# Optimization experiments

Hardware: AMD Instinct MI355X
Metric: run time of the kernel (lower is better)

## Reference

```python
import jax, jax.numpy as jnp
import numpy as np
from jax import lax

EPS = 1e-5
B, C, H, W = 16, 256, 56, 56
HEADS, DIM_K, DIM_U, DIM_OUT = 4, 16, 4, 256
DIM_V = DIM_OUT // HEADS  # 64
R = 15


def setup_inputs() -> dict:
    key = jax.random.key(0)
    ks = jax.random.split(key, 16)
    s = 0.05
    return {
        "x": jax.random.normal(ks[0], (B, C, H, W), jnp.float32),
        "Wq": jax.random.normal(ks[1], (C, HEADS * DIM_K), jnp.float32) * s,
        "Wk": jax.random.normal(ks[2], (C, DIM_U * DIM_K), jnp.float32) * s,
        "Wv": jax.random.normal(ks[3], (C, DIM_U * DIM_V), jnp.float32) * s,
        "pos_w": jax.random.normal(ks[4], (DIM_K, DIM_U, 1, R, R), jnp.float32) * s,
        "pos_b": jax.random.normal(ks[5], (DIM_K,), jnp.float32) * s,
        "gq": jax.random.uniform(ks[6], (HEADS * DIM_K,), jnp.float32),
        "bq": jax.random.normal(ks[7], (HEADS * DIM_K,), jnp.float32) * s,
        "mq": jax.random.normal(ks[8], (HEADS * DIM_K,), jnp.float32) * s,
        "vq": jax.random.uniform(ks[9], (HEADS * DIM_K,), jnp.float32) + 0.5,
        "gv": jax.random.uniform(ks[10], (DIM_U * DIM_V,), jnp.float32),
        "bv": jax.random.normal(ks[11], (DIM_U * DIM_V,), jnp.float32) * s,
        "mv": jax.random.normal(ks[12], (DIM_U * DIM_V,), jnp.float32) * s,
        "vv": jax.random.uniform(ks[13], (DIM_U * DIM_V,), jnp.float32) + 0.5,
    }


def _bn(x, gamma, beta, mean, var):
    # inference-mode BatchNorm over channel dim (axis=1), x: [b,c,h,w]
    inv = gamma / jnp.sqrt(var + EPS)
    return x * inv[None, :, None, None] + (beta - mean * inv)[None, :, None, None]


def reference(x, Wq, Wk, Wv, pos_w, pos_b, gq, bq, mq, vq, gv, bv, mv, vv):
    b, c, hh, ww = x.shape
    n = hh * ww
    h, dk, u, dv = HEADS, DIM_K, DIM_U, DIM_V
    # 1x1 convs (channels_first) == channel matmuls
    q = jnp.einsum('bchw,cd->bdhw', x, Wq)
    k = jnp.einsum('bchw,cd->bdhw', x, Wk)
    v = jnp.einsum('bchw,cd->bdhw', x, Wv)
    q = _bn(q, gq, bq, mq, vq)
    v = _bn(v, gv, bv, mv, vv)
    # rearranges: 'b (h k) hh ww -> b h k (hh ww)', 'b (u k) hh ww -> b u k n', 'b (u v) hh ww -> b u v n'
    q = q.reshape(b, h, dk, n)
    k = k.reshape(b, u, dk, n)
    v = v.reshape(b, u, dv, n)
    k = jax.nn.softmax(k, axis=-1)  # keras Softmax default axis=-1 (positions)
    # content lambda
    Lc = jnp.einsum('bukm,buvm->bkv', k, v)
    Yc = jnp.einsum('bhkn,bkv->bnhv', q, Lc)
    # position lambda: conv3d over (v,hh,ww) with kernel (1,r,r), pad spatial only
    v5 = v.reshape(b, u, dv, hh, ww)  # [N, C=u, D=v, H, W]
    p = R // 2
    Lp = lax.conv_general_dilated(
        v5, pos_w, window_strides=(1, 1, 1),
        padding=[(0, 0), (p, p), (p, p)],
        dimension_numbers=('NCDHW', 'OIDHW', 'NCDHW'))
    Lp = Lp + pos_b[None, :, None, None, None]  # [b, k, v, hh, ww]
    Lp = Lp.reshape(b, dk, dv, n)
    Yp = jnp.einsum('bhkn,bkvn->bnhv', q, Lp)
    Y = Yc + Yp  # [b, n, h, v]
    # 'b (hh ww) h v -> b (h v) hh ww'
    out = Y.reshape(b, hh, ww, h, dv).transpose(0, 3, 4, 1, 2).reshape(b, h * dv, hh, ww)
    return out
```

## Files before the change

kernel.cpp:

```cpp
#include <hip/hip_runtime.h>
#include <cstdint>
#include <cstddef>

#define NB   16
#define NC   256
#define NPIX 3136
#define NW   56
#define EPSV 1e-5f

#define BSTR     (384 * NPIX)
#define OFF_VP   (128 * NPIX)
#define VROWD    36
#define VPLANE   (56 * VROWD)
#define OFF_PARTB 917504

#define OFF_AB   0u
#define OFF_BNA  49152u
#define OFF_BNB  49536u
#define OFF_WT   49920u
#define OFF_KS   58112u
#define OFF_LC   59136u
#define OFF_Y    75520u

typedef short bf16x8 __attribute__((ext_vector_type(8)));
typedef float f32x4  __attribute__((ext_vector_type(4)));
typedef float f32x16 __attribute__((ext_vector_type(16)));

__device__ __forceinline__ uint32_t f2bf(float f) {
  uint32_t x = __float_as_uint(f);
  uint32_t r = x + 0x7fffu + ((x >> 16) & 1u);
  return r >> 16;
}
__device__ __forceinline__ uint32_t cvtpk(float lo, float hi) {
  uint32_t r;
  asm("v_cvt_pk_bf16_f32 %0, %1, %2" : "=v"(r) : "v"(lo), "v"(hi));
  return r;
}

__device__ __forceinline__ float fetchW(const float* Wq, const float* Wk,
                                        const float* Wv, int m, int c) {
  if (m < 64)  return Wq[c * 64 + m];
  if (m < 128) return Wk[c * 64 + (m - 64)];
  return Wv[c * 256 + (m - 128)];
}

__global__ void prep_kernel(const float* __restrict__ Wq, const float* __restrict__ Wk,
                            const float* __restrict__ Wv, const float* __restrict__ pos_w,
                            const float* __restrict__ gq, const float* __restrict__ bq,
                            const float* __restrict__ mq, const float* __restrict__ vq,
                            const float* __restrict__ gv, const float* __restrict__ bv,
                            const float* __restrict__ mv, const float* __restrict__ vv,
                            float* __restrict__ ws) {
  int d = blockIdx.x;
  int c = threadIdx.x;
  int i = d * 256 + c;
  if (i < 49152) {
    int dgt = i >> 12, rem = i & 4095;
    int kc = rem >> 8, rem2 = rem & 255;
    int lane = rem2 >> 2, dp = rem2 & 3;
    int m = dgt * 32 + (lane & 31);
    int k0 = kc * 16 + (lane >> 5) * 8 + dp * 2;
    float w0 = fetchW(Wq, Wk, Wv, m, k0);
    float w1 = fetchW(Wq, Wk, Wv, m, k0 + 1);
    ((uint32_t*)(ws + OFF_AB))[i] = f2bf(w0) | (f2bf(w1) << 16);
  }
  if (c == 0) {
    float sa, sb;
    if (d < 64)        { float inv = gq[d] / sqrtf(vq[d] + EPSV); sa = inv; sb = bq[d] - mq[d] * inv; }
    else if (d < 128)  { sa = 1.0f; sb = 0.0f; }
    else               { int j = d - 128; float inv = gv[j] / sqrtf(vv[j] + EPSV); sa = inv; sb = bv[j] - mv[j] * inv; }
    ws[OFF_BNA + d] = sa;
    ws[OFF_BNB + d] = sb;
  }
  if (i < 8192) {
    int chunk = i >> 8, rem = i & 255, lane = rem >> 2, dp = rem & 3;
    int quad = lane >> 4, k = lane & 15;
    int u = chunk >> 3, t = chunk & 7;
    int dh = 2 * t + (quad >> 1);
    int dwb = (quad & 1) * 8 + dp * 2;
    float w0 = (dh < 15 && dwb     < 15) ? pos_w[k * 900 + u * 225 + dh * 15 + dwb]     : 0.0f;
    float w1 = (dh < 15 && dwb + 1 < 15) ? pos_w[k * 900 + u * 225 + dh * 15 + dwb + 1] : 0.0f;
    ((uint32_t*)(ws + OFF_WT))[i] = f2bf(w0) | (f2bf(w1) << 16);
  }
  if (i < 1024) ws[OFF_KS + i] = 0.0f;
  for (int g = i; g < 4096 * 56; g += 98304) {
    int plane = g / 56, r = g - plane * 56;
    int bb = plane >> 8, d2 = plane & 255;
    uint32_t* row = (uint32_t*)(ws + OFF_Y) + (size_t)bb * BSTR + OFF_VP
                    + (size_t)d2 * VPLANE + r * VROWD;
    uint4 z; z.x = 0; z.y = 0; z.z = 0; z.w = 0;
    *(uint4*)(row)      = z;
    *(uint4*)(row + 32) = z;
  }
}

__launch_bounds__(256, 2)
__global__ void qkv_mfma(const float* __restrict__ x, const float* __restrict__ wsc,
                         float* __restrict__ Y) {
  __shared__ uint32_t X[64 * 128];
  __shared__ float BNs[768];
  int tid = threadIdx.x;
  int n0 = blockIdx.x * 64, b = blockIdx.y;
  for (int i = tid; i < 768; i += 256) BNs[i] = wsc[OFF_BNA + i];
  const size_t xb = (size_t)b * NC * NPIX;
#pragma unroll
  for (int it = 0; it < 4; ++it) {
    int n2 = tid & 31;
    int cp4 = it * 8 + (tid >> 5);
    const float* xp = x + xb + (size_t)(cp4 * 8) * NPIX + n0 + n2 * 2;
    float2 ld[8];
#pragma unroll
    for (int j = 0; j < 8; ++j) ld[j] = *(const float2*)(xp + (size_t)j * NPIX);
    uint4 ve, vo;
    ve.x = cvtpk(ld[0].x, ld[1].x);
    ve.y = cvtpk(ld[2].x, ld[3].x);
    ve.z = cvtpk(ld[4].x, ld[5].x);
    ve.w = cvtpk(ld[6].x, ld[7].x);
    vo.x = cvtpk(ld[0].y, ld[1].y);
    vo.y = cvtpk(ld[2].y, ld[3].y);
    vo.z = cvtpk(ld[4].y, ld[5].y);
    vo.w = cvtpk(ld[6].y, ld[7].y);
    int ne = 2 * n2, no = ne + 1;
    *(uint4*)(X + ne * 128 + ((cp4 ^ (ne & 31)) << 2)) = ve;
    *(uint4*)(X + no * 128 + ((cp4 ^ (no & 31)) << 2)) = vo;
  }
  __syncthreads();
  int lane = tid & 63, w = tid >> 6;
  int n31 = lane & 31, h5 = lane >> 5;
  f32x16 acc[3][2];
#pragma unroll
  for (int dt = 0; dt < 3; ++dt)
#pragma unroll
    for (int nt = 0; nt < 2; ++nt)
#pragma unroll
      for (int e = 0; e < 16; ++e) acc[dt][nt][e] = 0.0f;
  const uint4* AB = (const uint4*)(wsc + OFF_AB);
  if (w == 0) {
#pragma unroll 4
    for (int kc = 0; kc < 16; ++kc) {
      bf16x8 af[3];
#pragma unroll
      for (int dt = 0; dt < 3; ++dt) {
        union { uint4 q; bf16x8 v; } tmp;
        tmp.q = AB[(size_t)((dt * 16 + kc)) * 64 + lane];
        af[dt] = tmp.v;
      }
#pragma unroll
      for (int nt = 0; nt < 2; ++nt) {
        union { uint4 q; bf16x8 v; } bu;
        bu.q = *(const uint4*)(X + (nt * 32 + n31) * 128 + (((2 * kc + h5) ^ n31) << 2));
        acc[0][nt] = __builtin_amdgcn_mfma_f32_32x32x16_bf16(af[0], bu.v, acc[0][nt], 0, 0, 0);
        acc[1][nt] = __builtin_amdgcn_mfma_f32_32x32x16_bf16(af[1], bu.v, acc[1][nt], 0, 0, 0);
        acc[2][nt] = __builtin_amdgcn_mfma_f32_32x32x16_bf16(bu.v, af[2], acc[2][nt], 0, 0, 0);
      }
    }
  } else {
#pragma unroll 4
    for (int kc = 0; kc < 16; ++kc) {
      bf16x8 af[3];
#pragma unroll
      for (int dt = 0; dt < 3; ++dt) {
        union { uint4 q; bf16x8 v; } tmp;
        tmp.q = AB[(size_t)(((w * 3 + dt) * 16 + kc)) * 64 + lane];
        af[dt] = tmp.v;
      }
#pragma unroll
      for (int nt = 0; nt < 2; ++nt) {
        union { uint4 q; bf16x8 v; } bu;
        bu.q = *(const uint4*)(X + (nt * 32 + n31) * 128 + (((2 * kc + h5) ^ n31) << 2));
#pragma unroll
        for (int dt = 0; dt < 3; ++dt)
          acc[dt][nt] = __builtin_amdgcn_mfma_f32_32x32x16_bf16(bu.v, af[dt], acc[dt][nt], 0, 0, 0);
      }
    }
  }
  int prr[2][4], pcc[2][4];
#pragma unroll
  for (int nt = 0; nt < 2; ++nt)
#pragma unroll
    for (int j = 0; j < 4; ++j) {
      int pb = n0 + nt * 32 + 8 * j + 4 * h5;
      prr[nt][j] = pb / NW;
      pcc[nt][j] = pb - prr[nt][j] * NW;
    }
  if (w == 0) {
#pragma unroll
    for (int dt = 0; dt < 2; ++dt) {
      int dgt = dt;
      float sa[16], sb[16];
#pragma unroll
      for (int g = 0; g < 4; ++g) {
        *(float4*)(sa + g * 4) = *(const float4*)(BNs + dgt * 32 + g * 8 + h5 * 4);
        *(float4*)(sb + g * 4) = *(const float4*)(BNs + 384 + dgt * 32 + g * 8 + h5 * 4);
      }
#pragma unroll
      for (int nt = 0; nt < 2; ++nt) {
        int pix = n0 + nt * 32 + n31;
        uint2* qb2 = (uint2*)(Y + (size_t)b * BSTR);
#pragma unroll
        for (int g = 0; g < 4; ++g) {
          float y0 = fmaf(acc[dt][nt][4 * g + 0], sa[4 * g + 0], sb[4 * g + 0]);
          float y1 = fmaf(acc[dt][nt][4 * g + 1], sa[4 * g + 1], sb[4 * g + 1]);
          float y2 = fmaf(acc[dt][nt][4 * g + 2], sa[4 * g + 2], sb[4 * g + 2]);
          float y3 = fmaf(acc[dt][nt][4 * g + 3], sa[4 * g + 3], sb[4 * g + 3]);
          uint2 val;
          val.x = cvtpk(y0, y1);
          val.y = cvtpk(y2, y3);
          qb2[(size_t)(dgt * 8 + 2 * g + h5) * NPIX + pix] = val;
        }
      }
    }
    {
      float* kp = Y + ((size_t)(b * 384) + 64 + n31) * NPIX;
#pragma unroll
      for (int nt = 0; nt < 2; ++nt)
#pragma unroll
        for (int j = 0; j < 4; ++j) {
          float4 st;
          st.x = acc[2][nt][4 * j + 0];
          st.y = acc[2][nt][4 * j + 1];
          st.z = acc[2][nt][4 * j + 2];
          st.w = acc[2][nt][4 * j + 3];
          *(float4*)(kp + prr[nt][j] * NW + pcc[nt][j]) = st;
        }
    }
  } else {
    unsigned short* vp = (unsigned short*)(Y + (size_t)b * BSTR + OFF_VP);
#pragma unroll
    for (int dt = 0; dt < 3; ++dt) {
      int dgt = w * 3 + dt;
      if (dgt == 3) {
        float* kp = Y + ((size_t)(b * 384) + 96 + n31) * NPIX;
#pragma unroll
        for (int nt = 0; nt < 2; ++nt)
#pragma unroll
          for (int j = 0; j < 4; ++j) {
            float4 st;
            st.x = acc[dt][nt][4 * j + 0];
            st.y = acc[dt][nt][4 * j + 1];
            st.z = acc[dt][nt][4 * j + 2];
            st.w = acc[dt][nt][4 * j + 3];
            *(float4*)(kp + prr[nt][j] * NW + pcc[nt][j]) = st;
          }
      } else {
        int d2 = dgt * 32 + n31 - 128;
        float sa = BNs[dgt * 32 + n31];
        float sb2 = BNs[384 + dgt * 32 + n31];
        unsigned short* vpd = vp + (size_t)d2 * 4032;
#pragma unroll
        for (int nt = 0; nt < 2; ++nt)
#pragma unroll
          for (int j = 0; j < 4; ++j) {
            float y0 = fmaf(acc[dt][nt][4 * j + 0], sa, sb2);
            float y1 = fmaf(acc[dt][nt][4 * j + 1], sa, sb2);
            float y2 = fmaf(acc[dt][nt][4 * j + 2], sa, sb2);
            float y3 = fmaf(acc[dt][nt][4 * j + 3], sa, sb2);
            uint2 val;
            val.x = cvtpk(y0, y1);
            val.y = cvtpk(y2, y3);
            *(uint2*)(vpd + prr[nt][j] * 72 + 8 + pcc[nt][j]) = val;
          }
      }
    }
  }
}

__launch_bounds__(256)
__global__ void lc_mfma(float* __restrict__ Y, float* __restrict__ ws) {
  __shared__ float R[4096];
  __shared__ float Rs[64];
  int bx = blockIdx.x, u = blockIdx.y, b = blockIdx.z;
  int tid = threadIdx.x;
  int lane = tid & 63, w = tid >> 6;
  int col = lane & 15, quad = lane >> 4;
  int slot = bx * 4 + w;
  const float* krow = Y + ((size_t)(b * 384 + 64 + u * 16 + col)) * NPIX;
  const uint32_t* vpb = (const uint32_t*)(Y + (size_t)b * BSTR + OFF_VP)
                        + (size_t)(u * 64 + col) * VPLANE;
  f32x4 acc[4];
#pragma unroll
  for (int vt = 0; vt < 4; ++vt) acc[vt] = (f32x4){0.f, 0.f, 0.f, 0.f};
  float ssum = 0.0f;
  for (int c = slot; c < 126; c += 64) {
    int p0 = c * 32 + quad * 8;
    int row = p0 / 72;
    int pc = p0 - row * 72;
    bool valid = (unsigned)(pc - 8) < 56u;
    float4 k0, k1;
    if (valid) {
      const float* kp = krow + row * NW + pc - 8;
      k0 = *(const float4*)(kp);
      k1 = *(const float4*)(kp + 4);
    } else {
      k0.x = k0.y = k0.z = k0.w = -1e30f;
      k1 = k0;
    }
    float e0 = __expf(k0.x), e1 = __expf(k0.y), e2 = __expf(k0.z), e3 = __expf(k0.w);
    float e4 = __expf(k1.x), e5 = __expf(k1.y), e6 = __expf(k1.z), e7 = __expf(k1.w);
    ssum += (e0 + e1 + e2 + e3) + (e4 + e5 + e6 + e7);
    union { uint32_t d[4]; bf16x8 v; } kb;
    kb.d[0] = cvtpk(e0, e1);
    kb.d[1] = cvtpk(e2, e3);
    kb.d[2] = cvtpk(e4, e5);
    kb.d[3] = cvtpk(e6, e7);
    int vdw = c * 16 + quad * 4;
#pragma unroll
    for (int vt = 0; vt < 4; ++vt) {
      union { uint4 q; bf16x8 v; } vb;
      vb.q = *(const uint4*)(vpb + (size_t)(vt * 16) * VPLANE + vdw);
      acc[vt] = __builtin_amdgcn_mfma_f32_16x16x32_bf16(vb.v, kb.v, acc[vt], 0, 0, 0);
    }
  }
  ssum += __shfl_xor(ssum, 16);
  ssum += __shfl_xor(ssum, 32);
#pragma unroll
  for (int vt = 0; vt < 4; ++vt)
#pragma unroll
    for (int r = 0; r < 4; ++r)
      R[w * 1024 + vt * 256 + quad * 64 + r * 16 + col] = acc[vt][r];
  if (lane < 16) Rs[w * 16 + col] = ssum;
  __syncthreads();
  float* P = Y + (size_t)b * BSTR + OFF_PARTB + (size_t)(u * 16 + bx) * 1024;
  float4 s0 = *(const float4*)(R + tid * 4);
  float4 s1 = *(const float4*)(R + 1024 + tid * 4);
  float4 s2 = *(const float4*)(R + 2048 + tid * 4);
  float4 s3 = *(const float4*)(R + 3072 + tid * 4);
  float4 tot;
  tot.x = (s0.x + s1.x) + (s2.x + s3.x);
  tot.y = (s0.y + s1.y) + (s2.y + s3.y);
  tot.z = (s0.z + s1.z) + (s2.z + s3.z);
  tot.w = (s0.w + s1.w) + (s2.w + s3.w);
  *(float4*)(P + tid * 4) = tot;
  if (tid < 16)
    atomicAdd(&ws[OFF_KS + b * 64 + u * 16 + tid],
              (Rs[tid] + Rs[16 + tid]) + (Rs[32 + tid] + Rs[48 + tid]));
}

__global__ void lc_reduce(const float* __restrict__ Y, float* __restrict__ ws) {
  int i = blockIdx.x, b = blockIdx.y;
  int t = threadIdx.x;
  __shared__ float invS[64];
  if (t < 64) invS[t] = 1.0f / ws[OFF_KS + b * 64 + t];
  __syncthreads();
  int idx = i * 256 + t;
  int k = idx & 15;
  const float* P = Y + (size_t)b * BSTR + OFF_PARTB;
  float tot = 0.0f;
#pragma unroll
  for (int u = 0; u < 4; ++u) {
    float su = 0.0f;
#pragma unroll
    for (int s = 0; s < 16; ++s) su += P[(size_t)(u * 16 + s) * 1024 + idx];
    tot += su * invS[u * 16 + k];
  }
  ws[OFF_LC + (b * 16 + k) * 64 + (idx >> 4)] = tot;
}

#define ROWS    29
#define RSTR2   72
#define UPITCH2 2088
#define LDSW2   8352

template<int PPLO, int PPHI>
__device__ __forceinline__ void conv_accum(const uint32_t* __restrict__ S,
                                           const uint4* __restrict__ wt,
                                           int abase, int lane, f32x4* acc) {
#pragma unroll 1
  for (int u = 0; u < 4; ++u) {
    bf16x8 wf[8];
#pragma unroll
    for (int t = 0; t < 8; ++t) {
      union { uint4 q; bf16x8 v; } tmp;
      tmp.q = wt[(u * 8 + t) * 64 + lane];
      wf[t] = tmp.v;
    }
    int au = u * UPITCH2 + abase;
#pragma unroll
    for (int PP = PPLO; PP < PPHI; ++PP) {
      int a = au + PP * (2 * RSTR2);
      union { uint32_t u4[4]; bf16x8 v8; } bu;
      bu.u4[0] = S[a];     bu.u4[1] = S[a + 2];
      bu.u4[2] = S[a + 4]; bu.u4[3] = S[a + 6];
#pragma unroll
      for (int t = 0; t < 8; ++t) {
        int q = PP - t;
        if (q >= 0 && q < 7)
          acc[q] = __builtin_amdgcn_mfma_f32_16x16x32_bf16(wf[t], bu.v8, acc[q], 0, 0, 0);
      }
    }
  }
}

__launch_bounds__(512, 4)
__global__ void pos_lambda_mfma(const float* __restrict__ Y, const float* __restrict__ wsc,
                                const float* __restrict__ pos_b, float* __restrict__ out) {
  __shared__ __attribute__((aligned(16))) uint32_t S[LDSW2];
  int v = blockIdx.x, b = blockIdx.y, band = blockIdx.z;
  int rb = band * 14;
  int tid = threadIdx.x;
  const uint32_t* vpad = (const uint32_t*)(Y + (size_t)b * BSTR + OFF_VP);
  for (int ii = tid; ii < 1044; ii += 512) {
    int u = ii / 261;
    int rem = ii - u * 261;
    int row = rem / 9;
    int j3 = rem - row * 9;
    int gr = rb + row - 7;
    uint32_t d0 = 0, d1 = 0, d2 = 0, d3 = 0, d4 = 0;
    if ((unsigned)gr < (unsigned)NW) {
      const uint32_t* pr32 = vpad + (size_t)(u * 64 + v) * VPLANE + gr * VROWD + 4 * j3;
      uint4 q4 = *(const uint4*)pr32;
      d0 = q4.x; d1 = q4.y; d2 = q4.z; d3 = q4.w;
      d4 = pr32[4];
    }
    uint32_t* dst = S + u * UPITCH2 + row * RSTR2 + 8 * j3;
    uint4 w0, w1;
    w0.x = __builtin_amdgcn_alignbit(d1, d0, 16);  w0.y = d1;
    w0.z = __builtin_amdgcn_alignbit(d2, d1, 16);  w0.w = d2;
    w1.x = __builtin_amdgcn_alignbit(d3, d2, 16);  w1.y = d3;
    w1.z = __builtin_amdgcn_alignbit(d4, d3, 16);  w1.w = d4;
    *(uint4*)(dst)     = w0;
    *(uint4*)(dst + 4) = w1;
  }
  __syncthreads();
  int lane = tid & 63, wid = tid >> 6;
  int quad = lane >> 4, n = lane & 15;
  int dhp = quad >> 1;
  int ct = wid & 3, p = wid >> 2;
  int cb = (ct == 3) ? 40 : ct * 16;
  int sb = cb + n + (quad & 1) * 8;
  int abase = (p + dhp) * RSTR2 + sb;
  const uint4* wt = (const uint4*)(wsc + OFF_WT);
  float lcq[4];
#pragma unroll
  for (int r = 0; r < 4; ++r) {
    int k = quad * 4 + r;
    lcq[r] = wsc[OFF_LC + (b * 16 + k) * 64 + v] + pos_b[k];
  }
  f32x4 acc[7];
#pragma unroll
  for (int q = 0; q < 7; ++q) {
    acc[q][0] = lcq[0]; acc[q][1] = lcq[1]; acc[q][2] = lcq[2]; acc[q][3] = lcq[3];
  }
  if (band == 0)      conv_accum<3, 14>(S, wt, abase, lane, acc);
  else if (band == 3) conv_accum<0, 11>(S, wt, abase, lane, acc);
  else                conv_accum<0, 14>(S, wt, abase, lane, acc);

  const uint2* qb2 = (const uint2*)(Y + (size_t)b * BSTR);
#pragma unroll
  for (int q = 0; q < 7; ++q) {
    int rr = rb + p + 2 * q;
    int pix = rr * NW + cb + n;
    float m0 = acc[q][0], m1 = acc[q][1];
    float m2 = acc[q][2], m3 = acc[q][3];
    float pp[4];
#pragma unroll
    for (int j = 0; j < 4; ++j) {
      int h = quad ^ j;
      uint2 qd = qb2[(h * 4 + quad) * NPIX + pix];
      float q0 = __uint_as_float(qd.x << 16);
      float q1 = __uint_as_float(qd.x & 0xffff0000u);
      float q2 = __uint_as_float(qd.y << 16);
      float q3 = __uint_as_float(qd.y & 0xffff0000u);
      pp[j] = fmaf(q0, m0, fmaf(q1, m1, fmaf(q2, m2, q3 * m3)));
    }
    float t0 = pp[0] + __shfl_xor(pp[1], 16);
    float t2 = pp[2] + __shfl_xor(pp[3], 16);
    float y  = t0 + __shfl_xor(t2, 32);
    out[((size_t)(b * 256 + quad * 64 + v)) * NPIX + pix] = y;
  }
}

extern "C" void kernel_launch(void* const* d_in, const int* in_sizes, int n_in,
                              void* d_out, int out_size, void* d_ws, size_t ws_size,
                              hipStream_t stream) {
  const float* x     = (const float*)d_in[0];
  const float* Wq    = (const float*)d_in[1];
  const float* Wk    = (const float*)d_in[2];
  const float* Wv    = (const float*)d_in[3];
  const float* pos_w = (const float*)d_in[4];
  const float* pos_b = (const float*)d_in[5];
  const float* gq    = (const float*)d_in[6];
  const float* bq    = (const float*)d_in[7];
  const float* mq    = (const float*)d_in[8];
  const float* vq    = (const float*)d_in[9];
  const float* gv    = (const float*)d_in[10];
  const float* bv    = (const float*)d_in[11];
  const float* mv    = (const float*)d_in[12];
  const float* vv    = (const float*)d_in[13];
  float* ws  = (float*)d_ws;
  float* out = (float*)d_out;
  float* Y   = ws + OFF_Y;

  prep_kernel<<<dim3(384), 256, 0, stream>>>(Wq, Wk, Wv, pos_w, gq, bq, mq, vq,
                                             gv, bv, mv, vv, ws);
  qkv_mfma<<<dim3(49, 16), 256, 0, stream>>>(x, ws, Y);
  lc_mfma<<<dim3(16, 4, 16), 256, 0, stream>>>(Y, ws);
  lc_reduce<<<dim3(4, 16), 256, 0, stream>>>(Y, ws);
  pos_lambda_mfma<<<dim3(64, 16, 4), 512, 0, stream>>>(Y, ws, pos_b, out);
}
```

Baseline: 260.9 us.

## Fuse key exponentiation into QKV epilogue, store bf16 exp(k) in padded layout

The QKV projection epilogue now computes exp of the key logits and writes them as bf16 into a padded plane layout matching the value planes, replacing the fp32 key store. The content-lambda kernel then loads pre-exponentiated bf16 keys directly and computes the softmax denominator with an extra MFMA against a ones vector instead of scalar sums and shuffles. This halves key write/read traffic and removes exp work from the reduction kernel. The trade-offs are extra padding-zero initialization for the new planes and exp computed without max subtraction, now rounded to bf16 before summing.

```diff
diff --git a/kernel.cpp b/kernel.cpp
--- a/kernel.cpp
+++ b/kernel.cpp
@@ -9,6 +9,7 @@
 #define EPSV 1e-5f
 
 #define BSTR     (384 * NPIX)
+#define OFF_EK   (64 * NPIX)
 #define OFF_VP   (128 * NPIX)
 #define VROWD    36
 #define VPLANE   (56 * VROWD)
@@ -83,11 +84,12 @@
     ((uint32_t*)(ws + OFF_WT))[i] = f2bf(w0) | (f2bf(w1) << 16);
   }
   if (i < 1024) ws[OFF_KS + i] = 0.0f;
-  for (int g = i; g < 4096 * 56; g += 98304) {
+  for (int g = i; g < 5120 * 56; g += 98304) {
     int plane = g / 56, r = g - plane * 56;
-    int bb = plane >> 8, d2 = plane & 255;
-    uint32_t* row = (uint32_t*)(ws + OFF_Y) + (size_t)bb * BSTR + OFF_VP
-                    + (size_t)d2 * VPLANE + r * VROWD;
+    int bb = plane / 320, pl = plane - bb * 320;
+    size_t poff = (pl < 256) ? ((size_t)OFF_VP + (size_t)pl * VPLANE)
+                             : ((size_t)OFF_EK + (size_t)(pl - 256) * VPLANE);
+    uint32_t* row = (uint32_t*)(ws + OFF_Y) + (size_t)bb * BSTR + poff + r * VROWD;
     uint4 z; z.x = 0; z.y = 0; z.z = 0; z.w = 0;
     *(uint4*)(row)      = z;
     *(uint4*)(row + 32) = z;
@@ -183,6 +185,7 @@
       prr[nt][j] = pb / NW;
       pcc[nt][j] = pb - prr[nt][j] * NW;
     }
+  unsigned short* ekbase = (unsigned short*)(Y + (size_t)b * BSTR + OFF_EK);
   if (w == 0) {
 #pragma unroll
     for (int dt = 0; dt < 2; ++dt) {
@@ -211,17 +214,19 @@
       }
     }
     {
-      float* kp = Y + ((size_t)(b * 384) + 64 + n31) * NPIX;
+      unsigned short* ek = ekbase + (size_t)n31 * 4032;
 #pragma unroll
       for (int nt = 0; nt < 2; ++nt)
 #pragma unroll
         for (int j = 0; j < 4; ++j) {
-          float4 st;
-          st.x = acc[2][nt][4 * j + 0];
-          st.y = acc[2][nt][4 * j + 1];
-          st.z = acc[2][nt][4 * j + 2];
-          st.w = acc[2][nt][4 * j + 3];
-          *(float4*)(kp + prr[nt][j] * NW + pcc[nt][j]) = st;
+          float e0 = __expf(acc[2][nt][4 * j + 0]);
+          float e1 = __expf(acc[2][nt][4 * j + 1]);
+          float e2 = __expf(acc[2][nt][4 * j + 2]);
+          float e3 = __expf(acc[2][nt][4 * j + 3]);
+          uint2 val;
+          val.x = cvtpk(e0, e1);
+          val.y = cvtpk(e2, e3);
+          *(uint2*)(ek + prr[nt][j] * 72 + 8 + pcc[nt][j]) = val;
         }
     }
   } else {
@@ -230,17 +235,19 @@
     for (int dt = 0; dt < 3; ++dt) {
       int dgt = w * 3 + dt;
       if (dgt == 3) {
-        float* kp = Y + ((size_t)(b * 384) + 96 + n31) * NPIX;
+        unsigned short* ek = ekbase + (size_t)(32 + n31) * 4032;
 #pragma unroll
         for (int nt = 0; nt < 2; ++nt)
 #pragma unroll
           for (int j = 0; j < 4; ++j) {
-            float4 st;
-            st.x = acc[dt][nt][4 * j + 0];
-            st.y = acc[dt][nt][4 * j + 1];
-            st.z = acc[dt][nt][4 * j + 2];
-            st.w = acc[dt][nt][4 * j + 3];
-            *(float4*)(kp + prr[nt][j] * NW + pcc[nt][j]) = st;
+            float e0 = __expf(acc[dt][nt][4 * j + 0]);
+            float e1 = __expf(acc[dt][nt][4 * j + 1]);
+            float e2 = __expf(acc[dt][nt][4 * j + 2]);
+            float e3 = __expf(acc[dt][nt][4 * j + 3]);
+            uint2 val;
+            val.x = cvtpk(e0, e1);
+            val.y = cvtpk(e2, e3);
+            *(uint2*)(ek + prr[nt][j] * 72 + 8 + pcc[nt][j]) = val;
           }
       } else {
         int d2 = dgt * 32 + n31 - 128;
@@ -274,51 +281,36 @@
   int lane = tid & 63, w = tid >> 6;
   int col = lane & 15, quad = lane >> 4;
   int slot = bx * 4 + w;
-  const float* krow = Y + ((size_t)(b * 384 + 64 + u * 16 + col)) * NPIX;
+  const uint32_t* ekp = (const uint32_t*)(Y + (size_t)b * BSTR + OFF_EK)
+                        + (size_t)(u * 16 + col) * VPLANE;
   const uint32_t* vpb = (const uint32_t*)(Y + (size_t)b * BSTR + OFF_VP)
                         + (size_t)(u * 64 + col) * VPLANE;
+  bf16x8 ones;
+  { union { uint4 q; bf16x8 v; } o;
+    o.q.x = 0x3F803F80u; o.q.y = 0x3F803F80u; o.q.z = 0x3F803F80u; o.q.w = 0x3F803F80u;
+    ones = o.v; }
   f32x4 acc[4];
 #pragma unroll
   for (int vt = 0; vt < 4; ++vt) acc[vt] = (f32x4){0.f, 0.f, 0.f, 0.f};
-  float ssum = 0.0f;
+  f32x4 acc5 = (f32x4){0.f, 0.f, 0.f, 0.f};
   for (int c = slot; c < 126; c += 64) {
-    int p0 = c * 32 + quad * 8;
-    int row = p0 / 72;
-    int pc = p0 - row * 72;
-    bool valid = (unsigned)(pc - 8) < 56u;
-    float4 k0, k1;
-    if (valid) {
-      const float* kp = krow + row * NW + pc - 8;
-      k0 = *(const float4*)(kp);
-      k1 = *(const float4*)(kp + 4);
-    } else {
-      k0.x = k0.y = k0.z = k0.w = -1e30f;
-      k1 = k0;
-    }
-    float e0 = __expf(k0.x), e1 = __expf(k0.y), e2 = __expf(k0.z), e3 = __expf(k0.w);
-    float e4 = __expf(k1.x), e5 = __expf(k1.y), e6 = __expf(k1.z), e7 = __expf(k1.w);
-    ssum += (e0 + e1 + e2 + e3) + (e4 + e5 + e6 + e7);
-    union { uint32_t d[4]; bf16x8 v; } kb;
-    kb.d[0] = cvtpk(e0, e1);
-    kb.d[1] = cvtpk(e2, e3);
-    kb.d[2] = cvtpk(e4, e5);
-    kb.d[3] = cvtpk(e6, e7);
     int vdw = c * 16 + quad * 4;
+    union { uint4 q; bf16x8 v; } kb;
+    kb.q = *(const uint4*)(ekp + vdw);
 #pragma unroll
     for (int vt = 0; vt < 4; ++vt) {
       union { uint4 q; bf16x8 v; } vb;
       vb.q = *(const uint4*)(vpb + (size_t)(vt * 16) * VPLANE + vdw);
       acc[vt] = __builtin_amdgcn_mfma_f32_16x16x32_bf16(vb.v, kb.v, acc[vt], 0, 0, 0);
     }
-  }
-  ssum += __shfl_xor(ssum, 16);
-  ssum += __shfl_xor(ssum, 32);
+    acc5 = __builtin_amdgcn_mfma_f32_16x16x32_bf16(ones, kb.v, acc5, 0, 0, 0);
+  }
 #pragma unroll
   for (int vt = 0; vt < 4; ++vt)
 #pragma unroll
     for (int r = 0; r < 4; ++r)
       R[w * 1024 + vt * 256 + quad * 64 + r * 16 + col] = acc[vt][r];
-  if (lane < 16) Rs[w * 16 + col] = ssum;
+  if (lane < 16) Rs[w * 16 + col] = acc5[0];
   __syncthreads();
   float* P = Y + (size_t)b * BSTR + OFF_PARTB + (size_t)(u * 16 + bx) * 1024;
   float4 s0 = *(const float4*)(R + tid * 4);
```

New measurement: 263.3 us. About the same (+0.9%).
